# Kernel tuning notes

Hardware: AMD Instinct MI355X
Metric: run time of the kernel (lower is better)

Reference implementation:

```python
import jax, jax.numpy as jnp
import numpy as np

N_HEADS = 12

def setup_inputs() -> dict:
    key = jax.random.key(0)
    k1, k2, k3 = jax.random.split(key, 3)
    B, N, D = 2, 2048, 768
    x = jax.random.normal(k1, (B, N, D), dtype=jnp.float32)
    # Linear weights stored as [in, out] (equivalent to torch W.T)
    Wkqv = jax.random.normal(k2, (D, 3 * D), dtype=jnp.float32) * (1.0 / np.sqrt(D))
    bkqv = jnp.zeros((3 * D,), dtype=jnp.float32)
    Wproj = jax.random.normal(k3, (D, D), dtype=jnp.float32) * (1.0 / np.sqrt(D))
    bproj = jnp.zeros((D,), dtype=jnp.float32)
    return {"x": x, "Wkqv": Wkqv, "bkqv": bkqv, "Wproj": Wproj, "bproj": bproj}


def reference(x, Wkqv, bkqv, Wproj, bproj):
    B, N, D = x.shape
    H = N_HEADS
    hd = D // H
    kqv = x @ Wkqv + bkqv                     # [B, N, 3D]
    # NOTE: original chunks in (k, q, v) order
    k, q, v = jnp.split(kqv, 3, axis=-1)
    k = k.reshape(B, N, H, hd).transpose(0, 2, 1, 3)   # [B, H, N, hd]
    q = q.reshape(B, N, H, hd).transpose(0, 2, 1, 3)
    v = v.reshape(B, N, H, hd).transpose(0, 2, 1, 3)
    att = jnp.einsum('bhqd,bhkd->bhqk', q, k) / jnp.sqrt(jnp.float32(hd))
    causal = jnp.tril(jnp.ones((N, N), dtype=bool))    # [N, N]
    att = jnp.where(causal[None, None, :, :], att, jnp.float32(-jnp.inf))
    w = jax.nn.softmax(att, axis=-1)
    sa = jnp.einsum('bhqk,bhkd->bhqd', w, v)           # [B, H, N, hd]
    sa = sa.transpose(0, 2, 1, 3).reshape(B, N, D)
    return sa @ Wproj + bproj
```

## Files before the change

kernel.cpp:

```cpp
#include <hip/hip_runtime.h>

typedef __attribute__((ext_vector_type(8))) short bf16x8;
typedef __attribute__((ext_vector_type(4))) float f32x4;
typedef __attribute__((ext_vector_type(16))) float f32x16;

#define BATCH 2
#define SEQ 2048
#define DMODEL 768
#define NH 12
#define HD 64
#define M_TOK (BATCH * SEQ)
#define N_KQV (3 * DMODEL)

#define GLOAD16(gsrc, ldst) __builtin_amdgcn_global_load_lds( \
    (const __attribute__((address_space(1))) unsigned int*)(const void*)(gsrc), \
    (__attribute__((address_space(3))) unsigned int*)(void*)(ldst), 16, 0, 0)

__device__ __forceinline__ unsigned short f2bf(float f) {
  unsigned int u = __float_as_uint(f);
  u += 0x7FFFu + ((u >> 16) & 1u);
  return (unsigned short)(u >> 16);
}


__global__ void cvt_f32_bf16(const float* __restrict__ in,
                             unsigned short* __restrict__ out, int n4) {
  int i = blockIdx.x * blockDim.x + threadIdx.x;
  if (i >= n4) return;
  float4 v = reinterpret_cast<const float4*>(in)[i];
  unsigned long long p = (unsigned long long)f2bf(v.x)
                       | ((unsigned long long)f2bf(v.y) << 16)
                       | ((unsigned long long)f2bf(v.z) << 32)
                       | ((unsigned long long)f2bf(v.w) << 48);
  reinterpret_cast<unsigned long long*>(out)[i] = p;
}

__global__ void transpose_cvt(const float* __restrict__ in,
                              unsigned short* __restrict__ out,
                              int rows, int cols) {
  __shared__ float tile[32][33];
  int c0 = blockIdx.x * 32, r0 = blockIdx.y * 32;
  for (int i = threadIdx.y; i < 32; i += 8)
    tile[i][threadIdx.x] = in[(size_t)(r0 + i) * cols + c0 + threadIdx.x];
  __syncthreads();
  for (int i = threadIdx.y; i < 32; i += 8)
    out[(size_t)(c0 + i) * rows + r0 + threadIdx.x] = f2bf(tile[threadIdx.x][i]);
}

template <int MODE>
__global__ __launch_bounds__(256) void gemm_bt(
    const unsigned short* __restrict__ A,
    const unsigned short* __restrict__ BT,
    const float* __restrict__ bias,
    int M, int N, int K,
    unsigned short* __restrict__ outK, unsigned short* __restrict__ outQ,
    unsigned short* __restrict__ outVT, float* __restrict__ outF) {
  __shared__ __align__(16) unsigned short lds_a[2][128][32];
  __shared__ __align__(16) unsigned short lds_b[2][128][32];
  const int tid = threadIdx.x;
  const int lane = tid & 63;
  const int w = tid >> 6;
  const int wm = w >> 1, wn = w & 1;
  const int l15 = lane & 15, lg = lane >> 4;
  const int m0 = blockIdx.y * 128, n0 = blockIdx.x * 128;

  f32x4 acc[4][4];
#pragma unroll
  for (int i = 0; i < 4; i++)
#pragma unroll
    for (int jj = 0; jj < 4; jj++) acc[i][jj] = (f32x4){0.f, 0.f, 0.f, 0.f};

  const int grow = lane >> 2;
  const int gcol = (lane & 3) * 8;

  const int KT = K >> 5;

#define STAGE_TILE(buf, k0)                                                  \
  {                                                                          \
    const size_t a0 = (size_t)(m0 + w * 32 + grow) * K + (k0) + gcol;        \
    const size_t b0 = (size_t)(n0 + w * 32 + grow) * K + (k0) + gcol;        \
    GLOAD16(&A[a0],                  &lds_a[buf][w * 32][0]);                \
    GLOAD16(&A[a0 + 16 * (size_t)K], &lds_a[buf][w * 32 + 16][0]);           \
    GLOAD16(&BT[b0],                 &lds_b[buf][w * 32][0]);                \
    GLOAD16(&BT[b0 + 16 * (size_t)K], &lds_b[buf][w * 32 + 16][0]);          \
  }

  STAGE_TILE(0, 0);
  __syncthreads();

  for (int kt = 0; kt < KT; ++kt) {
    const int cur = kt & 1;
    if (kt + 1 < KT) STAGE_TILE(cur ^ 1, (kt + 1) << 5);
    bf16x8 af[4], bfr[4];
#pragma unroll
    for (int mi = 0; mi < 4; mi++)
      af[mi] = *(const bf16x8*)&lds_a[cur][wm * 64 + mi * 16 + l15][lg * 8];
#pragma unroll
    for (int ni = 0; ni < 4; ni++)
      bfr[ni] = *(const bf16x8*)&lds_b[cur][wn * 64 + ni * 16 + l15][lg * 8];
#pragma unroll
    for (int mi = 0; mi < 4; mi++)
#pragma unroll
      for (int ni = 0; ni < 4; ni++)
        acc[mi][ni] = __builtin_amdgcn_mfma_f32_16x16x32_bf16(af[mi], bfr[ni], acc[mi][ni], 0, 0, 0);
    __syncthreads();
  }
#undef STAGE_TILE

#pragma unroll
  for (int mi = 0; mi < 4; mi++) {
#pragma unroll
    for (int ni = 0; ni < 4; ni++) {
#pragma unroll
      for (int r = 0; r < 4; r++) {
        int row = m0 + wm * 64 + mi * 16 + lg * 4 + r;
        int col = n0 + wn * 64 + ni * 16 + l15;
        float v = acc[mi][ni][r] + bias[col];
        if (MODE == 0) {
          int chunk = col / DMODEL;
          int d = col - chunk * DMODEL;
          int hh = d >> 6, di = d & 63;
          int bb = row >> 11, tok = row & 2047;
          int bh = bb * NH + hh;
          if (chunk == 0)
            outK[((size_t)bh * SEQ + tok) * HD + di] = f2bf(v);
          else if (chunk == 1)
            outQ[((size_t)bh * SEQ + tok) * HD + di] = f2bf(v * 0.125f);
          else
            outVT[((size_t)bh * HD + di) * SEQ + tok] = f2bf(v);
        } else {
          outF[(size_t)row * N + col] = v;
        }
      }
    }
  }
}

__global__ __launch_bounds__(128) void attn_kernel(
    const unsigned short* __restrict__ qbuf,
    const unsigned short* __restrict__ kbuf,
    const unsigned short* __restrict__ vT,
    unsigned short* __restrict__ sa) {
  __shared__ __align__(16) unsigned short k_lds[64][72];
  __shared__ __align__(16) unsigned short v_lds[64][72];
  __shared__ __align__(16) unsigned short p_lds[2][32][40];
  __shared__ float o_merge[2][32][33];
  __shared__ float l_merge[2][32];
  const int tid = threadIdx.x, lane = tid & 63, w = tid >> 6;
  const int l31 = lane & 31, hi = lane >> 5;

  const int fid = (int)blockIdx.y * (int)gridDim.x + (int)blockIdx.x;
  const int xcd = fid & 7, slot = fid >> 3;
  const int bh = ((slot >> 6) << 3) + xcd;
  const int t = 63 - (slot & 63);
  const int ktmax = t >> 1;

  const size_t qk_base = (size_t)bh * SEQ * HD;
  const size_t v_base = (size_t)bh * HD * SEQ;
  const int bb = bh / NH, h = bh - bb * NH;

  const int sr = w * 32 + (lane >> 3);
  const int sc = (lane & 7) * 8;

  bf16x8 ones;
#pragma unroll
  for (int i = 0; i < 8; i++) ones[i] = (short)0x3F80;

  {
    bf16x8 rk[4], rv[4];
#pragma unroll
    for (int p = 0; p < 4; p++) {
      rk[p] = *(const bf16x8*)&kbuf[qk_base + (size_t)(sr + 8 * p) * HD + sc];
      rv[p] = *(const bf16x8*)&vT[v_base + (size_t)(sr + 8 * p) * SEQ + sc];
    }
#pragma unroll
    for (int p = 0; p < 4; p++) {
      *(bf16x8*)&k_lds[sr + 8 * p][sc] = rk[p];
      *(bf16x8*)&v_lds[sr + 8 * p][sc] = rv[p];
    }
  }

  bf16x8 aq[4];
#pragma unroll
  for (int ds = 0; ds < 4; ds++)
    aq[ds] = *(const bf16x8*)&qbuf[qk_base + (size_t)(t * 32 + l31) * HD + ds * 16 + hi * 8];

  f32x16 o0, o1, lacc;
#pragma unroll
  for (int i = 0; i < 16; i++) { o0[i] = 0.f; o1[i] = 0.f; lacc[i] = 0.f; }

  __syncthreads();

  for (int kt = 0; kt <= ktmax; ++kt) {
    const bool more = (kt < ktmax);
    bf16x8 rk[4], rv[4];
    if (more) {
      const int nrow = (kt + 1) * 64;
#pragma unroll
      for (int p = 0; p < 4; p++) {
        rk[p] = *(const bf16x8*)&kbuf[qk_base + (size_t)(nrow + sr + 8 * p) * HD + sc];
        rv[p] = *(const bf16x8*)&vT[v_base + (size_t)(sr + 8 * p) * SEQ + nrow + sc];
      }
    }

    f32x16 s;
#pragma unroll
    for (int i = 0; i < 16; i++) s[i] = 0.f;
    __builtin_amdgcn_s_setprio(1);
#pragma unroll
    for (int ds = 0; ds < 4; ds++) {
      bf16x8 bk = *(const bf16x8*)&k_lds[w * 32 + l31][ds * 16 + hi * 8];
      s = __builtin_amdgcn_mfma_f32_32x32x16_bf16(aq[ds], bk, s, 0, 0, 0);
    }
    __builtin_amdgcn_s_setprio(0);

    const bool diag = (kt == ktmax);
    const int qbase = (t & 1) * 32;
#pragma unroll
    for (int r = 0; r < 16; r++) {
      int ql = (r & 3) + 8 * (r >> 2) + 4 * hi;
      float val = s[r];
      if (diag && (w * 32 + l31 > qbase + ql)) val = -1e30f;
      p_lds[w][ql][l31] = f2bf(__expf(val));
    }

    __builtin_amdgcn_s_setprio(1);
#pragma unroll
    for (int kc = 0; kc < 2; kc++) {
      bf16x8 ap = *(const bf16x8*)&p_lds[w][l31][kc * 16 + hi * 8];
      lacc = __builtin_amdgcn_mfma_f32_32x32x16_bf16(ap, ones, lacc, 0, 0, 0);
      bf16x8 bv0 = *(const bf16x8*)&v_lds[l31][w * 32 + kc * 16 + hi * 8];
      o0 = __builtin_amdgcn_mfma_f32_32x32x16_bf16(ap, bv0, o0, 0, 0, 0);
      bf16x8 bv1 = *(const bf16x8*)&v_lds[32 + l31][w * 32 + kc * 16 + hi * 8];
      o1 = __builtin_amdgcn_mfma_f32_32x32x16_bf16(ap, bv1, o1, 0, 0, 0);
    }
    __builtin_amdgcn_s_setprio(0);

    if (more) {
      __syncthreads();
#pragma unroll
      for (int p = 0; p < 4; p++) {
        *(bf16x8*)&k_lds[sr + 8 * p][sc] = rk[p];
        *(bf16x8*)&v_lds[sr + 8 * p][sc] = rv[p];
      }
      __syncthreads();
    }
  }

  {
    f32x16 osend = w ? o0 : o1;
#pragma unroll
    for (int r = 0; r < 16; r++) {
      int ql = (r & 3) + 8 * (r >> 2) + 4 * hi;
      o_merge[w][ql][l31] = osend[r];
      if (l31 == 0) l_merge[w][ql] = lacc[r];
    }
    __syncthreads();
    f32x16 okeep = w ? o1 : o0;
#pragma unroll
    for (int r = 0; r < 16; r++) {
      int ql = (r & 3) + 8 * (r >> 2) + 4 * hi;
      float ot = okeep[r] + o_merge[1 - w][ql][l31];
      float lt = lacc[r] + l_merge[1 - w][ql];
      sa[((size_t)bb * SEQ + t * 32 + ql) * DMODEL + h * HD + w * 32 + l31] = f2bf(ot / lt);
    }
  }
}


extern "C" void kernel_launch(void* const* d_in, const int* in_sizes, int n_in,
                              void* d_out, int out_size, void* d_ws, size_t ws_size,
                              hipStream_t stream) {
  const float* x     = (const float*)d_in[0];
  const float* Wkqv  = (const float*)d_in[1];
  const float* bkqv  = (const float*)d_in[2];
  const float* Wproj = (const float*)d_in[3];
  const float* bproj = (const float*)d_in[4];
  float* out = (float*)d_out;

  char* ws = (char*)d_ws;
  unsigned short* x_bf   = (unsigned short*)(ws + 0);
  unsigned short* wkqvT  = (unsigned short*)(ws + 6291456);
  unsigned short* wprojT = (unsigned short*)(ws + 9830400);
  unsigned short* qb     = (unsigned short*)(ws + 11010048);
  unsigned short* kb     = (unsigned short*)(ws + 17301504);
  unsigned short* vT     = (unsigned short*)(ws + 23592960);
  unsigned short* sa     = (unsigned short*)(ws + 29884416);

  cvt_f32_bf16<<<(M_TOK * DMODEL / 4 + 255) / 256, 256, 0, stream>>>(x, x_bf, M_TOK * DMODEL / 4);
  transpose_cvt<<<dim3(N_KQV / 32, DMODEL / 32), dim3(32, 8), 0, stream>>>(Wkqv, wkqvT, DMODEL, N_KQV);
  transpose_cvt<<<dim3(DMODEL / 32, DMODEL / 32), dim3(32, 8), 0, stream>>>(Wproj, wprojT, DMODEL, DMODEL);

  gemm_bt<0><<<dim3(N_KQV / 128, M_TOK / 128), 256, 0, stream>>>(
      x_bf, wkqvT, bkqv, M_TOK, N_KQV, DMODEL, kb, qb, vT, nullptr);

  attn_kernel<<<dim3(64, BATCH * NH), 128, 0, stream>>>(qb, kb, vT, sa);

  gemm_bt<1><<<dim3(DMODEL / 128, M_TOK / 128), 256, 0, stream>>>(
      sa, wprojT, bproj, M_TOK, DMODEL, DMODEL, nullptr, nullptr, nullptr, out);
}
```

Baseline: 116.3 us.

## Keep softmax probabilities in registers via transposed QK and permlane swaps

Swaps the MFMA operand order so the score tile comes out transposed, which lets each lane convert its probabilities to packed bf16 and rearrange them with permlane32_swap straight into the A-operand layout for the PV MFMA. This removes the p_lds shared-memory round trip. The row-sum is now accumulated with scalar adds plus a cross-lane shuffle instead of an extra MFMA against a vector of ones. The merge buffers alias the K/V LDS region, which needs an added barrier and relies on the register fragment layout being correct.

```diff
diff --git a/kernel.cpp b/kernel.cpp
--- a/kernel.cpp
+++ b/kernel.cpp
@@ -20,6 +20,12 @@
   unsigned int u = __float_as_uint(f);
   u += 0x7FFFu + ((u >> 16) & 1u);
   return (unsigned short)(u >> 16);
+}
+
+__device__ __forceinline__ unsigned int cvtpk(float lo, float hi) {
+  unsigned int r;
+  asm("v_cvt_pk_bf16_f32 %0, %1, %2" : "=v"(r) : "v"(lo), "v"(hi));
+  return r;
 }
 
 
@@ -141,11 +147,12 @@
     const unsigned short* __restrict__ kbuf,
     const unsigned short* __restrict__ vT,
     unsigned short* __restrict__ sa) {
-  __shared__ __align__(16) unsigned short k_lds[64][72];
-  __shared__ __align__(16) unsigned short v_lds[64][72];
-  __shared__ __align__(16) unsigned short p_lds[2][32][40];
-  __shared__ float o_merge[2][32][33];
-  __shared__ float l_merge[2][32];
+  __shared__ __align__(16) char smem_raw[18432];
+  auto k_lds = reinterpret_cast<unsigned short (*)[72]>(smem_raw);
+  auto v_lds = reinterpret_cast<unsigned short (*)[72]>(smem_raw + 9216);
+  auto o_merge = reinterpret_cast<float (*)[32][33]>(smem_raw);
+  auto l_merge = reinterpret_cast<float (*)[32]>(smem_raw + 9216);
+
   const int tid = threadIdx.x, lane = tid & 63, w = tid >> 6;
   const int l31 = lane & 31, hi = lane >> 5;
 
@@ -162,10 +169,6 @@
   const int sr = w * 32 + (lane >> 3);
   const int sc = (lane & 7) * 8;
 
-  bf16x8 ones;
-#pragma unroll
-  for (int i = 0; i < 8; i++) ones[i] = (short)0x3F80;
-
   {
     bf16x8 rk[4], rv[4];
 #pragma unroll
@@ -185,9 +188,10 @@
   for (int ds = 0; ds < 4; ds++)
     aq[ds] = *(const bf16x8*)&qbuf[qk_base + (size_t)(t * 32 + l31) * HD + ds * 16 + hi * 8];
 
-  f32x16 o0, o1, lacc;
-#pragma unroll
-  for (int i = 0; i < 16; i++) { o0[i] = 0.f; o1[i] = 0.f; lacc[i] = 0.f; }
+  f32x16 o0, o1;
+#pragma unroll
+  for (int i = 0; i < 16; i++) { o0[i] = 0.f; o1[i] = 0.f; }
+  float lsum = 0.f;
 
   __syncthreads();
 
@@ -210,29 +214,46 @@
 #pragma unroll
     for (int ds = 0; ds < 4; ds++) {
       bf16x8 bk = *(const bf16x8*)&k_lds[w * 32 + l31][ds * 16 + hi * 8];
-      s = __builtin_amdgcn_mfma_f32_32x32x16_bf16(aq[ds], bk, s, 0, 0, 0);
+      s = __builtin_amdgcn_mfma_f32_32x32x16_bf16(bk, aq[ds], s, 0, 0, 0);
     }
     __builtin_amdgcn_s_setprio(0);
 
     const bool diag = (kt == ktmax);
-    const int qbase = (t & 1) * 32;
+    const int qb2 = (t & 1) * 32;
 #pragma unroll
     for (int r = 0; r < 16; r++) {
-      int ql = (r & 3) + 8 * (r >> 2) + 4 * hi;
+      int kr = (r & 3) + 8 * (r >> 2) + 4 * hi;
       float val = s[r];
-      if (diag && (w * 32 + l31 > qbase + ql)) val = -1e30f;
-      p_lds[w][ql][l31] = f2bf(__expf(val));
+      if (diag && (w * 32 + kr > qb2 + l31)) val = -1e30f;
+      float p = __expf(val);
+      s[r] = p;
+      lsum += p;
+    }
+
+    union { unsigned int u[4]; bf16x8 v; } f1, f2;
+    {
+      unsigned int A = cvtpk(s[0], s[1]), B = cvtpk(s[2], s[3]);
+      unsigned int C = cvtpk(s[4], s[5]), D = cvtpk(s[6], s[7]);
+      auto rAC = __builtin_amdgcn_permlane32_swap(A, C, false, false);
+      auto rBD = __builtin_amdgcn_permlane32_swap(B, D, false, false);
+      f1.u[0] = rAC[0]; f1.u[1] = rBD[0]; f1.u[2] = rAC[1]; f1.u[3] = rBD[1];
+      unsigned int A2 = cvtpk(s[8], s[9]),   B2 = cvtpk(s[10], s[11]);
+      unsigned int C2 = cvtpk(s[12], s[13]), D2 = cvtpk(s[14], s[15]);
+      auto rAC2 = __builtin_amdgcn_permlane32_swap(A2, C2, false, false);
+      auto rBD2 = __builtin_amdgcn_permlane32_swap(B2, D2, false, false);
+      f2.u[0] = rAC2[0]; f2.u[1] = rBD2[0]; f2.u[2] = rAC2[1]; f2.u[3] = rBD2[1];
     }
 
     __builtin_amdgcn_s_setprio(1);
-#pragma unroll
-    for (int kc = 0; kc < 2; kc++) {
-      bf16x8 ap = *(const bf16x8*)&p_lds[w][l31][kc * 16 + hi * 8];
-      lacc = __builtin_amdgcn_mfma_f32_32x32x16_bf16(ap, ones, lacc, 0, 0, 0);
-      bf16x8 bv0 = *(const bf16x8*)&v_lds[l31][w * 32 + kc * 16 + hi * 8];
-      o0 = __builtin_amdgcn_mfma_f32_32x32x16_bf16(ap, bv0, o0, 0, 0, 0);
-      bf16x8 bv1 = *(const bf16x8*)&v_lds[32 + l31][w * 32 + kc * 16 + hi * 8];
-      o1 = __builtin_amdgcn_mfma_f32_32x32x16_bf16(ap, bv1, o1, 0, 0, 0);
+    {
+      bf16x8 bv00 = *(const bf16x8*)&v_lds[l31][w * 32 + hi * 8];
+      bf16x8 bv01 = *(const bf16x8*)&v_lds[32 + l31][w * 32 + hi * 8];
+      o0 = __builtin_amdgcn_mfma_f32_32x32x16_bf16(f1.v, bv00, o0, 0, 0, 0);
+      o1 = __builtin_amdgcn_mfma_f32_32x32x16_bf16(f1.v, bv01, o1, 0, 0, 0);
+      bf16x8 bv10 = *(const bf16x8*)&v_lds[l31][w * 32 + 16 + hi * 8];
+      bf16x8 bv11 = *(const bf16x8*)&v_lds[32 + l31][w * 32 + 16 + hi * 8];
+      o0 = __builtin_amdgcn_mfma_f32_32x32x16_bf16(f2.v, bv10, o0, 0, 0, 0);
+      o1 = __builtin_amdgcn_mfma_f32_32x32x16_bf16(f2.v, bv11, o1, 0, 0, 0);
     }
     __builtin_amdgcn_s_setprio(0);
 
@@ -247,13 +268,15 @@
     }
   }
 
+  __syncthreads();
   {
+    float ltot = lsum + __shfl_xor(lsum, 32);
+    if (hi == 0) l_merge[w][l31] = ltot;
     f32x16 osend = w ? o0 : o1;
 #pragma unroll
     for (int r = 0; r < 16; r++) {
       int ql = (r & 3) + 8 * (r >> 2) + 4 * hi;
       o_merge[w][ql][l31] = osend[r];
-      if (l31 == 0) l_merge[w][ql] = lacc[r];
     }
     __syncthreads();
     f32x16 okeep = w ? o1 : o0;
@@ -261,7 +284,7 @@
     for (int r = 0; r < 16; r++) {
       int ql = (r & 3) + 8 * (r >> 2) + 4 * hi;
       float ot = okeep[r] + o_merge[1 - w][ql][l31];
-      float lt = lacc[r] + l_merge[1 - w][ql];
+      float lt = l_merge[0][ql] + l_merge[1][ql];
       sa[((size_t)bb * SEQ + t * 32 + ql) * DMODEL + h * HD + w * 32 + l31] = f2bf(ot / lt);
     }
   }
```

Result: faster. 113.2 us (-2.6%).
